# Kernel optimization log

Hardware: AMD Instinct MI355X
Metric: run time of the kernel (lower is better)

Reference implementation:

```python
import jax, jax.numpy as jnp
import numpy as np

B, T, D = 2, 2048, 2048
H = 16
DK = 64          # head_k_dim (key_dim = D*0.5 = 1024)
DV = 128         # head_v_dim (value_dim = D*1.0 = 2048)
R = 16           # gate_low_rank_dim
GLN = 16.0       # gate_logit_normalizer
C = 64           # chunk size
EPS = 1e-5


def setup_inputs() -> dict:
    key = jax.random.key(0)
    ks = jax.random.split(key, 12)
    s = 0.02
    return {
        "hidden_states": jax.random.normal(ks[0], (B, T, D), jnp.float32),
        "Wq": jax.random.normal(ks[1], (D, H * DK), jnp.float32) * s,
        "Wk": jax.random.normal(ks[2], (D, H * DK), jnp.float32) * s,
        "Wv": jax.random.normal(ks[3], (D, H * DV), jnp.float32) * s,
        "Wgk1": jax.random.normal(ks[4], (D, R), jnp.float32) * s,
        "Wgk2": jax.random.normal(ks[5], (R, H * DK), jnp.float32) * s,
        "bgk2": jnp.zeros((H * DK,), jnp.float32),
        "Wg1": jax.random.normal(ks[6], (D, R), jnp.float32) * s,
        "Wg2": jax.random.normal(ks[7], (R, H * DV), jnp.float32) * s,
        "bg2": jnp.zeros((H * DV,), jnp.float32),
        "Wo": jax.random.normal(ks[8], (H * DV, D), jnp.float32) * s,
        "gnorm_w": jnp.ones((DV,), jnp.float32),
    }


def _gla_chunk(q, k, v, gk):
    """Chunked gated linear attention.
    q,k,gk: [B,T,H,DK], v: [B,T,H,DV]. Recurrence:
    S_t = diag(exp(gk_t)) S_{t-1} + k_t v_t^T ; o_t = q_t @ S_t.
    """
    nC = T // C
    # [nC, B, H, C, d]
    def to_chunks(x):
        return x.reshape(B, nC, C, H, -1).transpose(1, 0, 3, 2, 4)
    qc, kc, vc, gkc = map(to_chunks, (q, k, v, gk))
    Gc = jnp.cumsum(gkc, axis=3)  # inclusive cumsum of log-decays within chunk
    tri = jnp.tril(jnp.ones((C, C), bool))

    def step(S, inp):
        q_c, k_c, v_c, G_c = inp  # [B,H,C,dk] / [B,H,C,dv]
        qg = q_c * jnp.exp(G_c)            # decays <= 0 within chunk -> safe
        kg = k_c * jnp.exp(-G_c)
        # inter-chunk: state contribution
        o = jnp.einsum('bhcd,bhde->bhce', qg, S)
        # intra-chunk causal attention with decay
        A = jnp.einsum('bhid,bhjd->bhij', qg, kg)
        A = jnp.where(tri, A, 0.0)
        o = o + jnp.einsum('bhij,bhje->bhie', A, v_c)
        # state update
        G_last = G_c[:, :, -1, :]                       # [B,H,dk]
        k_dec = k_c * jnp.exp(G_last[:, :, None, :] - G_c)
        S = S * jnp.exp(G_last)[:, :, :, None] + jnp.einsum('bhcd,bhce->bhde', k_dec, v_c)
        return S, o

    S0 = jnp.zeros((B, H, DK, DV), q.dtype)
    _, o = jax.lax.scan(step, S0, (qc, kc, vc, Gc))
    # [nC,B,H,C,dv] -> [B,T,H,dv]
    return o.transpose(1, 0, 3, 2, 4).reshape(B, T, H, DV)


def reference(hidden_states, Wq, Wk, Wv, Wgk1, Wgk2, bgk2, Wg1, Wg2, bg2, Wo, gnorm_w):
    hs = hidden_states
    q = jax.nn.silu(hs @ Wq).reshape(B, T, H, DK)
    k = jax.nn.silu(hs @ Wk).reshape(B, T, H, DK)
    v = jax.nn.silu(hs @ Wv).reshape(B, T, H, DV)
    gk = ((hs @ Wgk1) @ Wgk2 + bgk2).reshape(B, T, H, DK)
    gk = jax.nn.log_sigmoid(gk) / GLN
    q = q * (DK ** -0.5)  # fla default scale
    o = _gla_chunk(q, k, v, gk)  # [B,T,H,DV]
    # RMSNorm over head_v_dim
    o = o * jax.lax.rsqrt(jnp.mean(o * o, axis=-1, keepdims=True) + EPS) * gnorm_w
    g = ((hs @ Wg1) @ Wg2 + bg2).reshape(B, T, H, DV)
    o = o * jax.nn.sigmoid(g)
    return o.reshape(B, T, H * DV) @ Wo
```

## Files before the change

kernel.cpp:

```cpp
#include <hip/hip_runtime.h>
#include <cstdint>

#define Bq   2
#define Tq   2048
#define Dq   2048
#define Hq   16
#define DKq  64
#define DVq  128
#define Cq   64
#define NCq  32
#define Mq   4096
#define NBH  32

typedef _Float16 f16;
typedef f16 f16x4 __attribute__((ext_vector_type(4)));
typedef f16 f16x8 __attribute__((ext_vector_type(8)));
typedef float f32x4 __attribute__((ext_vector_type(4)));
typedef unsigned short u16;
typedef u16 u16x8 __attribute__((ext_vector_type(8)));

__device__ __forceinline__ void gl_lds16(const void* g, void* l) {
    __builtin_amdgcn_global_load_lds(
        (const __attribute__((address_space(1))) uint32_t*)g,
        (__attribute__((address_space(3))) uint32_t*)l, 16, 0, 0);
}

#define BARX()   asm volatile("s_barrier" ::: "memory")
#define LGKM0()  asm volatile("s_waitcnt lgkmcnt(0)" ::: "memory")
#define VMW8()   asm volatile("s_waitcnt vmcnt(8)" ::: "memory")
#define VMW6()   asm volatile("s_waitcnt vmcnt(6)" ::: "memory")

__global__ __launch_bounds__(256) void trans_all(const float* __restrict__ Wq,
                                                 const float* __restrict__ Wk,
                                                 const float* __restrict__ Wv,
                                                 const float* __restrict__ Wo,
                                                 f16* __restrict__ Qkv, f16* __restrict__ WoT) {
    __shared__ float sh[4096];
    int blk = blockIdx.x;
    int tid = threadIdx.x;
    const float* W; f16* Dh; int N, nt, kt; long rowoff;
    if (blk < 2048)      { W = Wq; N = 1024; int t = blk;        nt = t & 31; kt = t >> 5; Dh = Qkv; rowoff = 0; }
    else if (blk < 4096) { W = Wk; N = 1024; int t = blk - 2048; nt = t & 31; kt = t >> 5; Dh = Qkv; rowoff = 1024; }
    else if (blk < 8192) { W = Wv; N = 2048; int t = blk - 4096; nt = t & 63; kt = t >> 6; Dh = Qkv; rowoff = 2048; }
    else                 { W = Wo; N = 2048; int t = blk - 8192; nt = t & 63; kt = t >> 6; Dh = WoT; rowoff = 0; }
    int tx = tid & 31, ty = tid >> 5;
#pragma unroll
    for (int i = 0; i < 4; i++) {
        int k = kt * 32 + ty + i * 8;
        int n = nt * 32 + tx;
        sh[tx * 33 + ty + i * 8] = W[(long)k * N + n];
    }
    __syncthreads();
#pragma unroll
    for (int i = 0; i < 4; i++) {
        int n = nt * 32 + ty + i * 8;
        int k = kt * 32 + tx;
        Dh[(rowoff + n) * 2048L + k] = (f16)sh[(ty + i * 8) * 33 + tx];
    }
}

__global__ __launch_bounds__(256) void hs_conv(const float* __restrict__ in,
                                               f16* __restrict__ out) {
    long i = ((long)blockIdx.x * 256 + threadIdx.x) * 8;
    float4 a = *(const float4*)(in + i);
    float4 b = *(const float4*)(in + i + 4);
    f16x8 h;
    h[0] = (f16)a.x; h[1] = (f16)a.y; h[2] = (f16)a.z; h[3] = (f16)a.w;
    h[4] = (f16)b.x; h[5] = (f16)b.y; h[6] = (f16)b.z; h[7] = (f16)b.w;
    *(f16x8*)(out + i) = h;
}

__global__ __launch_bounds__(256) void lowrank_tg(const float* __restrict__ hs,
                                                  const float* __restrict__ Wgk1,
                                                  const float* __restrict__ Wg1,
                                                  float* __restrict__ t_gk,
                                                  float* __restrict__ t_g) {
    __shared__ float sW[512 * 32];
    int tid = threadIdx.x;
    int blk = blockIdx.x;
    int r = tid >> 4, seg = tid & 15;
    long row = (long)blk * 16 + r;
    float acc[32];
#pragma unroll
    for (int c = 0; c < 32; c++) acc[c] = 0.f;
    for (int kc = 0; kc < 2048; kc += 512) {
        __syncthreads();
#pragma unroll
        for (int i = 0; i < 16; i++) {
            int s = tid + i * 256;
            int k = s >> 3, q = s & 7;
            float4 w = (q < 4) ? *(const float4*)(Wgk1 + (long)(kc + k) * 16 + q * 4)
                               : *(const float4*)(Wg1  + (long)(kc + k) * 16 + (q - 4) * 4);
            int qs = q ^ ((k >> 5) & 7);
            *(float4*)&sW[k * 32 + qs * 4] = w;
        }
        __syncthreads();
        const float* hp = hs + row * 2048 + kc + seg * 32;
        int xr = seg & 7;
#pragma unroll
        for (int k4 = 0; k4 < 8; k4++) {
            float4 hv = *(const float4*)(hp + k4 * 4);
            float hvv[4] = {hv.x, hv.y, hv.z, hv.w};
#pragma unroll
            for (int u = 0; u < 4; u++) {
                int k = seg * 32 + k4 * 4 + u;
                const float* wr = &sW[k * 32];
#pragma unroll
                for (int q = 0; q < 8; q++) {
                    float4 wv = *(const float4*)(wr + ((q ^ xr) * 4));
                    acc[q * 4 + 0] += hvv[u] * wv.x;
                    acc[q * 4 + 1] += hvv[u] * wv.y;
                    acc[q * 4 + 2] += hvv[u] * wv.z;
                    acc[q * 4 + 3] += hvv[u] * wv.w;
                }
            }
        }
    }
#pragma unroll
    for (int c = 0; c < 32; c++) {
        acc[c] += __shfl_xor(acc[c], 1);
        acc[c] += __shfl_xor(acc[c], 2);
        acc[c] += __shfl_xor(acc[c], 4);
        acc[c] += __shfl_xor(acc[c], 8);
    }
    if (seg == 0) {
        float4 a;
        a.x = acc[0];  a.y = acc[1];  a.z = acc[2];  a.w = acc[3];  *(float4*)(t_gk + row * 16)     = a;
        a.x = acc[4];  a.y = acc[5];  a.z = acc[6];  a.w = acc[7];  *(float4*)(t_gk + row * 16 + 4) = a;
        a.x = acc[8];  a.y = acc[9];  a.z = acc[10]; a.w = acc[11]; *(float4*)(t_gk + row * 16 + 8) = a;
        a.x = acc[12]; a.y = acc[13]; a.z = acc[14]; a.w = acc[15]; *(float4*)(t_gk + row * 16 + 12)= a;
        a.x = acc[16]; a.y = acc[17]; a.z = acc[18]; a.w = acc[19]; *(float4*)(t_g + row * 16)      = a;
        a.x = acc[20]; a.y = acc[21]; a.z = acc[22]; a.w = acc[23]; *(float4*)(t_g + row * 16 + 4)  = a;
        a.x = acc[24]; a.y = acc[25]; a.z = acc[26]; a.w = acc[27]; *(float4*)(t_g + row * 16 + 8)  = a;
        a.x = acc[28]; a.y = acc[29]; a.z = acc[30]; a.w = acc[31]; *(float4*)(t_g + row * 16 + 12) = a;
    }
}

__global__ __launch_bounds__(512, 2) void gemm256q(const f16* __restrict__ A,
                                                   const f16* __restrict__ Bt,
                                                   f16* __restrict__ h0,
                                                   f16* __restrict__ h1,
                                                   f16* __restrict__ h2) {
    __shared__ __align__(16) f16 sA[2][16384];
    __shared__ __align__(16) f16 sB[2][16384];
    int tid = threadIdx.x;
    int wave = tid >> 6, lane = tid & 63;
    int quad = lane >> 4, l16 = lane & 15;
    int wm = wave >> 2, wn = wave & 3;

    int cpx = (int)gridDim.x >> 3;
    int wid = ((int)blockIdx.x & 7) * cpx + ((int)blockIdx.x >> 3);
    int bm = wid & 15, bn = wid >> 4;

    const f16* Ab = A  + (long)bm * 256 * 2048;
    const f16* Bb = Bt + (long)bn * 256 * 2048;

    int srow = tid >> 3;
    int gsrc = ((tid & 7) ^ (srow & 7)) * 8;
    const f16* Asrc = Ab + (long)srow * 2048 + gsrc;
    const f16* Bsrc = Bb + (long)srow * 2048 + gsrc;

#define STAGE(P, KT) do { \
    const f16* as_ = Asrc + (KT) * 64; \
    const f16* bs_ = Bsrc + (KT) * 64; \
    f16* la_ = &sA[P][tid * 8]; \
    f16* lb_ = &sB[P][tid * 8]; \
    _Pragma("unroll") \
    for (int q_ = 0; q_ < 4; q_++) gl_lds16(as_ + (long)q_ * 64 * 2048, la_ + q_ * 4096); \
    _Pragma("unroll") \
    for (int q_ = 0; q_ < 4; q_++) gl_lds16(bs_ + (long)q_ * 64 * 2048, lb_ + q_ * 4096); \
} while (0)

    int go0 = (quad ^ (l16 & 7)) * 8;
    int go1 = go0 ^ 32;
    const f16* aB0 = &sA[0][(wm * 128 + l16) * 64];
    const f16* aB1 = &sA[1][(wm * 128 + l16) * 64];
    const f16* bB0 = &sB[0][(wn * 64 + l16) * 64];
    const f16* bB1 = &sB[1][(wn * 64 + l16) * 64];

    f16x8 afr[4][2], bfr[2][2][2];
    f32x4 acc[8][4] = {};

#define LDA(PB, MH) do { \
    _Pragma("unroll") \
    for (int ii_ = 0; ii_ < 4; ii_++) { \
        afr[ii_][0] = *(const f16x8*)(PB + ((MH) * 4 + ii_) * 1024 + go0); \
        afr[ii_][1] = *(const f16x8*)(PB + ((MH) * 4 + ii_) * 1024 + go1); \
    } \
} while (0)

#define LDB(PB, NH) do { \
    _Pragma("unroll") \
    for (int jj_ = 0; jj_ < 2; jj_++) { \
        bfr[NH][jj_][0] = *(const f16x8*)(PB + ((NH) * 2 + jj_) * 1024 + go0); \
        bfr[NH][jj_][1] = *(const f16x8*)(PB + ((NH) * 2 + jj_) * 1024 + go1); \
    } \
} while (0)

#define QMFMA(MH, NH) do { \
    __builtin_amdgcn_s_setprio(1); \
    _Pragma("unroll") \
    for (int ii_ = 0; ii_ < 4; ii_++) \
    _Pragma("unroll") \
    for (int jj_ = 0; jj_ < 2; jj_++) { \
        acc[(MH)*4+ii_][(NH)*2+jj_] = __builtin_amdgcn_mfma_f32_16x16x32_f16(afr[ii_][0], bfr[NH][jj_][0], acc[(MH)*4+ii_][(NH)*2+jj_], 0, 0, 0); \
        acc[(MH)*4+ii_][(NH)*2+jj_] = __builtin_amdgcn_mfma_f32_16x16x32_f16(afr[ii_][1], bfr[NH][jj_][1], acc[(MH)*4+ii_][(NH)*2+jj_], 0, 0, 0); \
    } \
    __builtin_amdgcn_s_setprio(0); \
} while (0)

    STAGE(0, 0);
    STAGE(1, 1);
    VMW8();
    BARX();

#pragma unroll 1
    for (int it = 0; it < 16; it++) {
        int kt2 = 2 * it + 2; if (kt2 > 31) kt2 = 31;
        int kt3 = 2 * it + 3; if (kt3 > 31) kt3 = 31;
        LDA(aB0, 0); LDB(bB0, 0);
        BARX(); LGKM0(); QMFMA(0, 0); BARX();
        LDB(bB0, 1);
        BARX(); LGKM0(); QMFMA(0, 1); BARX();
        LDA(aB0, 1);
        BARX(); LGKM0(); QMFMA(1, 0); BARX();
        STAGE(0, kt2);
        VMW8();
        BARX(); QMFMA(1, 1); BARX();
        LDA(aB1, 0); LDB(bB1, 0);
        BARX(); LGKM0(); QMFMA(0, 0); BARX();
        LDB(bB1, 1);
        BARX(); LGKM0(); QMFMA(0, 1); BARX();
        LDA(aB1, 1);
        BARX(); LGKM0(); QMFMA(1, 0); BARX();
        STAGE(1, kt3);
        VMW8();
        BARX(); QMFMA(1, 1); BARX();
    }
    asm volatile("s_waitcnt vmcnt(0)" ::: "memory");

    long rb = (long)bm * 256 + wm * 128 + quad * 4;
    f16* dst; long cw, cb; float sc = 1.f;
    if (bn < 4)      { dst = h0; cw = 1024; cb = (long)bn * 256;       sc = 0.125f; }
    else if (bn < 8) { dst = h1; cw = 1024; cb = (long)(bn - 4) * 256; }
    else             { dst = h2; cw = 2048; cb = (long)(bn - 8) * 256; }
    long cbase = cb + wn * 64 + l16;
#pragma unroll
    for (int i = 0; i < 8; i++)
#pragma unroll
        for (int j = 0; j < 4; j++)
#pragma unroll
            for (int r = 0; r < 4; r++) {
                float x = acc[i][j][r];
                x = x / (1.f + __expf(-x)) * sc;
                dst[(rb + i * 16 + r) * cw + cbase + j * 16] = (f16)x;
            }
#undef STAGE
#undef LDA
#undef LDB
#undef QMFMA
}

__global__ __launch_bounds__(512, 2) void gemm128o(const f16* __restrict__ A,
                                                   const f16* __restrict__ Bt,
                                                   float* __restrict__ o0) {
    __shared__ __align__(16) f16 sAb[16384];
    __shared__ __align__(16) f16 sBb[32768];
    int tid = threadIdx.x;
    int wave = tid >> 6, lane = tid & 63;
    int quad = lane >> 4, l16 = lane & 15;
    int wm = wave >> 2, wn = wave & 3;

    int cpx = (int)gridDim.x >> 3;
    int wid = ((int)blockIdx.x & 7) * cpx + ((int)blockIdx.x >> 3);
    int bm = wid & 31, bn = wid >> 5;

    int srow = tid >> 3;
    int gsrc = ((tid & 7) ^ (srow & 7)) * 8;
    const f16* Asrc = A  + ((long)bm * 128 + srow) * 2048 + gsrc;
    const f16* Bsrc = Bt + ((long)bn * 256 + srow) * 2048 + gsrc;

#define STAGE(P, KT) do { \
    _Pragma("unroll") \
    for (int q_ = 0; q_ < 2; q_++) \
        gl_lds16(Asrc + (KT) * 64 + (long)q_ * 64 * 2048, sAb + (P) * 8192 + tid * 8 + q_ * 4096); \
    _Pragma("unroll") \
    for (int q_ = 0; q_ < 4; q_++) \
        gl_lds16(Bsrc + (KT) * 64 + (long)q_ * 64 * 2048, sBb + (P) * 16384 + tid * 8 + q_ * 4096); \
} while (0)

    int go0 = (quad ^ (l16 & 7)) * 8;
    int go1 = go0 ^ 32;
    const f16* pA0 = sAb + (wm * 64 + l16) * 64 + go0;
    const f16* pA1 = sAb + (wm * 64 + l16) * 64 + go1;
    const f16* pB0 = sBb + (wn * 64 + l16) * 64 + go0;
    const f16* pB1 = sBb + (wn * 64 + l16) * 64 + go1;

    f16x8 aX[4], bX[4], aY[4], bY[4];
    f32x4 acc[4][4] = {};

#define RDA(D, PTR, POFF) do { \
    D[0] = *(const f16x8*)((PTR) + (POFF)); \
    D[1] = *(const f16x8*)((PTR) + (POFF) + 1024); \
    D[2] = *(const f16x8*)((PTR) + (POFF) + 2048); \
    D[3] = *(const f16x8*)((PTR) + (POFF) + 3072); \
} while (0)

#define MM(AS, BS) do { \
    __builtin_amdgcn_s_setprio(1); \
    _Pragma("unroll") \
    for (int m_ = 0; m_ < 4; m_++) \
    _Pragma("unroll") \
    for (int n_ = 0; n_ < 4; n_++) \
        acc[m_][n_] = __builtin_amdgcn_mfma_f32_16x16x32_f16(AS[m_], BS[n_], acc[m_][n_], 0, 0, 0); \
    __builtin_amdgcn_s_setprio(0); \
} while (0)

    STAGE(0, 0);
    STAGE(1, 1);
    VMW6();
    BARX();
    RDA(aX, pA0, 0); RDA(bX, pB0, 0);

#pragma unroll 1
    for (int it = 0; it < 16; it++) {
        int c2 = 2 * it + 2; if (c2 > 31) c2 = 31;
        int c3 = 2 * it + 3; if (c3 > 31) c3 = 31;
        RDA(aY, pA1, 0); RDA(bY, pB1, 0);
        MM(aX, bX);
        LGKM0();
        BARX();
        STAGE(0, c2);
        VMW6();
        BARX();
        RDA(aX, pA0, 8192); RDA(bX, pB0, 16384);
        MM(aY, bY);
        RDA(aY, pA1, 8192); RDA(bY, pB1, 16384);
        MM(aX, bX);
        LGKM0();
        BARX();
        STAGE(1, c3);
        VMW6();
        BARX();
        RDA(aX, pA0, 0); RDA(bX, pB0, 0);
        MM(aY, bY);
    }
    asm volatile("s_waitcnt vmcnt(0)" ::: "memory");

    long rb = (long)bm * 128 + wm * 64 + quad * 4;
    long cbase = (long)bn * 256 + wn * 64 + l16;
#pragma unroll
    for (int m = 0; m < 4; m++)
#pragma unroll
        for (int n = 0; n < 4; n++)
#pragma unroll
            for (int r = 0; r < 4; r++)
                o0[(rb + m * 16 + r) * 2048 + cbase + n * 16] = acc[m][n][r];
#undef STAGE
#undef RDA
#undef MM
}

__global__ __launch_bounds__(256) void vtrans(const u16* __restrict__ v,
                                              u16* __restrict__ vT) {
    __shared__ uint32_t su[128 * 65];
    int tid = threadIdx.x;
    int t0 = (blockIdx.x >> 5) * 128;
    int e0 = (blockIdx.x & 31) * 64;
#pragma unroll
    for (int i = 0; i < 4; i++) {
        int tr = i * 32 + (tid >> 3);
        int ec = (tid & 7) * 8;
        u16x8 g = *(const u16x8*)(v + (long)(t0 + tr) * 2048 + e0 + ec);
#pragma unroll
        for (int j = 0; j < 8; j++) su[tr * 65 + ec + j] = g[j];
    }
    __syncthreads();
#pragma unroll
    for (int i = 0; i < 2; i++) {
        int er = i * 32 + (tid >> 3);
        int tch = (tid & 7) * 16;
        u16x8 o0, o1;
#pragma unroll
        for (int j = 0; j < 8; j++) {
            o0[j] = (u16)su[(tch + j) * 65 + er];
            o1[j] = (u16)su[(tch + 8 + j) * 65 + er];
        }
        u16* dst = vT + (long)(e0 + er) * 4096 + t0 + tch;
        *(u16x8*)dst = o0;
        *(u16x8*)(dst + 8) = o1;
    }
}

__global__ __launch_bounds__(256) void gk_cum(const float* __restrict__ t_gk,
                                              const float* __restrict__ Wgk2,
                                              const float* __restrict__ bgk2,
                                              float* __restrict__ G,
                                              float* __restrict__ dec) {
    __shared__ float sT[1024];
    __shared__ float sW[1024];
    __shared__ float sb[64];
    __shared__ float sG[64 * 64];
    int blk = blockIdx.x;
    int c = blk & 31, h = (blk >> 5) & 15, b = blk >> 9;
    int tid = threadIdx.x;
    long rowbase = (long)b * Tq + c * 64;
    {
        int idx = tid * 4;
        *(float4*)&sT[idx] = *(const float4*)(t_gk + rowbase * 16 + idx);
        int rr = idx >> 6, dd = idx & 63;
        *(float4*)&sW[idx] = *(const float4*)(Wgk2 + rr * 1024 + h * 64 + dd);
    }
    if (tid < 64) sb[tid] = bgk2[h * 64 + tid];
    __syncthreads();
    int tquad = tid >> 4, dgrp = tid & 15;
    float4 bg4 = *(float4*)&sb[dgrp * 4];
#pragma unroll
    for (int j = 0; j < 4; j++) {
        int t = tquad * 4 + j;
        float4 z = bg4;
#pragma unroll
        for (int rr = 0; rr < 16; rr++) {
            float tv = sT[t * 16 + rr];
            float4 wv = *(float4*)&sW[rr * 64 + dgrp * 4];
            z.x += tv * wv.x; z.y += tv * wv.y; z.z += tv * wv.z; z.w += tv * wv.w;
        }
        float4 o;
        o.x = (fminf(z.x, 0.f) - log1pf(__expf(-fabsf(z.x)))) * 0.0625f;
        o.y = (fminf(z.y, 0.f) - log1pf(__expf(-fabsf(z.y)))) * 0.0625f;
        o.z = (fminf(z.z, 0.f) - log1pf(__expf(-fabsf(z.z)))) * 0.0625f;
        o.w = (fminf(z.w, 0.f) - log1pf(__expf(-fabsf(z.w)))) * 0.0625f;
        *(float4*)&sG[t * 64 + dgrp * 4] = o;
    }
    __syncthreads();
    if (tid < 64) {
        float run = 0.f;
        for (int t = 0; t < 64; t++) { run += sG[t * 64 + tid]; sG[t * 64 + tid] = run; }
        dec[blk * 64 + tid] = __expf(run);
    }
    __syncthreads();
    float* Gb = G + (long)blk * 4096;
#pragma unroll
    for (int i = 0; i < 4; i++) {
        int f = tid + i * 256;
        *(float4*)(Gb + f * 4) = *(float4*)&sG[f * 4];
    }
}

#define ST 68
__global__ __launch_bounds__(256) void gla_pass1(const f16* __restrict__ kbuf,
                                                 const f16* __restrict__ vh,
                                                 const float* __restrict__ G,
                                                 float* __restrict__ U) {
    __shared__ float sG[64 * ST];
    __shared__ float sK[64 * ST];
    int blk = blockIdx.x;
    int c = blk & 31, h = (blk >> 5) & 15, b = blk >> 9;
    int tid = threadIdx.x;
    long rowbase = (long)b * Tq + c * 64;
    const float* Gb = G + (long)blk * 4096;
#pragma unroll
    for (int i = 0; i < 4; i++) {
        int f = tid + i * 256;
        float4 v = *(const float4*)(Gb + f * 4);
        int t = f >> 4, d0 = (f & 15) * 4;
        *(float4*)&sG[t * ST + d0] = v;
    }
    __syncthreads();
#pragma unroll
    for (int i = 0; i < 16; i++) {
        int idx = tid + i * 256;
        int t = idx >> 6, d = idx & 63;
        float gl = sG[63 * ST + d];
        sK[t * ST + d] = (float)kbuf[(rowbase + t) * 1024 + h * 64 + d] * __expf(gl - sG[t * ST + d]);
    }
    __syncthreads();
    int ty = tid >> 4, tx = tid & 15;
    float acc[4][8] = {};
    const f16* vb = vh + rowbase * 2048 + h * 128 + tx * 8;
    for (int t = 0; t < 64; t++) {
        float kd[4];
        *(float4*)&kd[0] = *(float4*)&sK[t * ST + ty * 4];
        f16x8 vv = *(const f16x8*)(vb + (long)t * 2048);
        float ve[8];
#pragma unroll
        for (int e = 0; e < 8; e++) ve[e] = (float)vv[e];
#pragma unroll
        for (int r = 0; r < 4; r++)
#pragma unroll
            for (int e = 0; e < 8; e++) acc[r][e] += kd[r] * ve[e];
    }
    float* Ub = U + (long)blk * 8192;
#pragma unroll
    for (int r = 0; r < 4; r++) {
        int d = ty * 4 + r;
#pragma unroll
        for (int e8 = 0; e8 < 8; e8++)
            Ub[(tx * 8 + e8) * 64 + d] = acc[r][e8];
    }
}

__global__ __launch_bounds__(256) void gla_pass2(const float* __restrict__ U,
                                                 const float* __restrict__ dec,
                                                 f16* __restrict__ ShT) {
    int bh = blockIdx.x >> 2;
    int tid = threadIdx.x;
    int e = (blockIdx.x & 3) * 32 + (tid >> 3);
    int d0 = (tid & 7) * 8;
    float4 Sa = {0.f, 0.f, 0.f, 0.f}, Sb = {0.f, 0.f, 0.f, 0.f};
    for (int c = 0; c < NCq; c++) {
        long base = ((long)(bh * 32 + c) * 128 + e) * 64 + d0;
        float4 u0 = *(const float4*)(U + base);
        float4 u1 = *(const float4*)(U + base + 4);
        const float* dp = dec + (bh * 32 + c) * 64 + d0;
        float4 dc0 = *(const float4*)dp;
        float4 dc1 = *(const float4*)(dp + 4);
        f16x8 sh;
        sh[0] = (f16)Sa.x; sh[1] = (f16)Sa.y; sh[2] = (f16)Sa.z; sh[3] = (f16)Sa.w;
        sh[4] = (f16)Sb.x; sh[5] = (f16)Sb.y; sh[6] = (f16)Sb.z; sh[7] = (f16)Sb.w;
        *(f16x8*)(ShT + base) = sh;
        Sa.x = Sa.x * dc0.x + u0.x; Sa.y = Sa.y * dc0.y + u0.y;
        Sa.z = Sa.z * dc0.z + u0.z; Sa.w = Sa.w * dc0.w + u0.w;
        Sb.x = Sb.x * dc1.x + u1.x; Sb.y = Sb.y * dc1.y + u1.y;
        Sb.z = Sb.z * dc1.z + u1.z; Sb.w = Sb.w * dc1.w + u1.w;
    }
}

#define GRD(row, kslot) (((row) << 6) + ((((kslot) ^ ((row) & 7))) << 3))
__global__ __launch_bounds__(256) void gla_pass3(const f16* __restrict__ qb,
                                                 const f16* __restrict__ kb,
                                                 const float* __restrict__ G,
                                                 const float* __restrict__ t_g,
                                                 const float* __restrict__ Wg2,
                                                 const float* __restrict__ bg2,
                                                 const float* __restrict__ gnw,
                                                 const f16* __restrict__ ShT,
                                                 const f16* __restrict__ vT,
                                                 f16* __restrict__ Oh) {
    __shared__ __align__(16) f16 sQg[4096];
    __shared__ __align__(16) f16 sKg[4096];
    __shared__ __align__(16) f16 sAh[4096];
    __shared__ __align__(16) f16 sST[8192];
    __shared__ __align__(16) f16 sVT[8192];
    __shared__ float sWg[16 * 128];
    __shared__ float sbg[128];
    int blk = blockIdx.x;
    int c = blk & 31, h = (blk >> 5) & 15, b = blk >> 9;
    int tid = threadIdx.x;
    long rowbase = (long)b * Tq + c * 64;

#pragma unroll
    for (int i = 0; i < 4; i++) {
        int s = tid + i * 256;
        int e = s >> 3, gp = s & 7;
        int gl = gp ^ (e & 7);
        gl_lds16(ShT + (long)blk * 8192 + e * 64 + gl * 8, sST + s * 8);
        gl_lds16(vT + (long)(h * 128 + e) * 4096 + rowbase + gl * 8, sVT + s * 8);
    }
#pragma unroll
    for (int i = 0; i < 2; i++) {
        int idx = tid * 4 + i * 1024;
        int rr = idx >> 7, ee = idx & 127;
        *(float4*)&sWg[idx] = *(const float4*)(Wg2 + (long)rr * 2048 + h * 128 + ee);
    }
    if (tid < 128) sbg[tid] = bg2[h * 128 + tid];
#pragma unroll
    for (int i = 0; i < 4; i++) {
        int f = tid + i * 256;
        int t = f >> 4, gi = f & 15;
        float4 G4 = *(const float4*)(G + (long)blk * 4096 + f * 4);
        long gb = (rowbase + t) * 1024 + h * 64 + gi * 4;
        f16x4 q4 = *(const f16x4*)(qb + gb);
        f16x4 k4 = *(const f16x4*)(kb + gb);
        f16x4 qh, kh;
        float ex;
        ex = __expf(G4.x); qh[0] = (f16)((float)q4[0] * ex); kh[0] = (f16)((float)k4[0] / ex);
        ex = __expf(G4.y); qh[1] = (f16)((float)q4[1] * ex); kh[1] = (f16)((float)k4[1] / ex);
        ex = __expf(G4.z); qh[2] = (f16)((float)q4[2] * ex); kh[2] = (f16)((float)k4[2] / ex);
        ex = __expf(G4.w); qh[3] = (f16)((float)q4[3] * ex); kh[3] = (f16)((float)k4[3] / ex);
        int w = (t << 6) + ((((gi >> 1) ^ (t & 7))) << 3) + ((gi & 1) << 2);
        *(f16x4*)(sQg + w) = qh;
        *(f16x4*)(sKg + w) = kh;
    }
    __syncthreads();

    int wv = tid >> 6, lane = tid & 63;
    int quad = lane >> 4, l16 = lane & 15;
    int trow = wv * 16 + l16;

    f16x8 afq[2];
    afq[0] = *(const f16x8*)(sQg + GRD(trow, quad));
    afq[1] = *(const f16x8*)(sQg + GRD(trow, 4 + quad));
#pragma unroll
    for (int j4 = 0; j4 < 4; j4++) {
        int tc = j4 * 16 + l16;
        f16x8 bk0 = *(const f16x8*)(sKg + GRD(tc, quad));
        f16x8 bk1 = *(const f16x8*)(sKg + GRD(tc, 4 + quad));
        f32x4 ca = {};
        ca = __builtin_amdgcn_mfma_f32_16x16x32_f16(afq[0], bk0, ca, 0, 0, 0);
        ca = __builtin_amdgcn_mfma_f32_16x16x32_f16(afq[1], bk1, ca, 0, 0, 0);
#pragma unroll
        for (int r = 0; r < 4; r++) {
            int tr = wv * 16 + quad * 4 + r;
            int tcw = j4 * 16 + l16;
            f16 av = (tcw <= tr) ? (f16)ca[r] : (f16)0.f;
            sAh[(tr << 6) + ((((tcw >> 3) ^ (tr & 7))) << 3) + (tcw & 7)] = av;
        }
    }

    f16x8 afa[2];
    afa[0] = *(const f16x8*)(sAh + GRD(trow, quad));
    afa[1] = *(const f16x8*)(sAh + GRD(trow, 4 + quad));
    f32x4 acc[8];
#pragma unroll
    for (int et = 0; et < 8; et++) {
        int e = et * 16 + l16;
        f16x8 bs0 = *(const f16x8*)(sST + GRD(e, quad));
        f16x8 bs1 = *(const f16x8*)(sST + GRD(e, 4 + quad));
        f16x8 bv0 = *(const f16x8*)(sVT + GRD(e, quad));
        f16x8 bv1 = *(const f16x8*)(sVT + GRD(e, 4 + quad));
        f32x4 cc = {};
        cc = __builtin_amdgcn_mfma_f32_16x16x32_f16(afq[0], bs0, cc, 0, 0, 0);
        cc = __builtin_amdgcn_mfma_f32_16x16x32_f16(afq[1], bs1, cc, 0, 0, 0);
        cc = __builtin_amdgcn_mfma_f32_16x16x32_f16(afa[0], bv0, cc, 0, 0, 0);
        cc = __builtin_amdgcn_mfma_f32_16x16x32_f16(afa[1], bv1, cc, 0, 0, 0);
        acc[et] = cc;
    }

    float gw[8], bgv[8];
#pragma unroll
    for (int et = 0; et < 8; et++) {
        gw[et]  = gnw[et * 16 + l16];
        bgv[et] = sbg[et * 16 + l16];
    }
#pragma unroll
    for (int half = 0; half < 2; half++) {
        float tg[2][16];
#pragma unroll
        for (int rh = 0; rh < 2; rh++) {
            int t = wv * 16 + quad * 4 + half * 2 + rh;
            const float* tgp = t_g + (rowbase + t) * 16;
#pragma unroll
            for (int q4 = 0; q4 < 4; q4++)
                *(float4*)&tg[rh][q4 * 4] = *(const float4*)(tgp + q4 * 4);
        }
        float g[2][8];
#pragma unroll
        for (int rh = 0; rh < 2; rh++)
#pragma unroll
            for (int et = 0; et < 8; et++) g[rh][et] = bgv[et];
#pragma unroll
        for (int rr = 0; rr < 16; rr++) {
#pragma unroll
            for (int et = 0; et < 8; et++) {
                float wv_ = sWg[rr * 128 + et * 16 + l16];
                g[0][et] += tg[0][rr] * wv_;
                g[1][et] += tg[1][rr] * wv_;
            }
        }
#pragma unroll
        for (int rh = 0; rh < 2; rh++) {
            int r = half * 2 + rh;
            int t = wv * 16 + quad * 4 + r;
            float ss = 0.f;
#pragma unroll
            for (int et = 0; et < 8; et++) ss += acc[et][r] * acc[et][r];
            ss += __shfl_xor(ss, 1);
            ss += __shfl_xor(ss, 2);
            ss += __shfl_xor(ss, 4);
            ss += __shfl_xor(ss, 8);
            float scale = rsqrtf(ss * (1.f / 128.f) + 1e-5f);
            long off = (rowbase + t) * 2048 + h * 128 + l16;
#pragma unroll
            for (int et = 0; et < 8; et++) {
                float y = acc[et][r] * scale * gw[et] / (1.f + __expf(-g[rh][et]));
                Oh[off + et * 16] = (f16)y;
            }
        }
    }
}

extern "C" void kernel_launch(void* const* d_in, const int* in_sizes, int n_in,
                              void* d_out, int out_size, void* d_ws, size_t ws_size,
                              hipStream_t stream) {
    const float* hs   = (const float*)d_in[0];
    const float* Wq   = (const float*)d_in[1];
    const float* Wk   = (const float*)d_in[2];
    const float* Wv   = (const float*)d_in[3];
    const float* Wgk1 = (const float*)d_in[4];
    const float* Wgk2 = (const float*)d_in[5];
    const float* bgk2 = (const float*)d_in[6];
    const float* Wg1  = (const float*)d_in[7];
    const float* Wg2  = (const float*)d_in[8];
    const float* bg2  = (const float*)d_in[9];
    const float* Wo   = (const float*)d_in[10];
    const float* gnw  = (const float*)d_in[11];

    char* w = (char*)d_ws;
    auto alloc = [&](size_t bytes) {
        char* p = w; w += (bytes + 255) & ~size_t(255); return (void*)p;
    };
    f16*   Xh     = (f16*)  alloc((size_t)Mq * Dq * 2);
    f16*   WqkvT  = (f16*)  alloc((size_t)4224 * 2048 * 2);
    f16*   WoT    = (f16*)  alloc((size_t)2048 * 2048 * 2);
    f16*   qb     = (f16*)  alloc((size_t)Mq * 1024 * 2);
    f16*   kb     = (f16*)  alloc((size_t)Mq * 1024 * 2);
    f16*   vhb    = (f16*)  alloc((size_t)Mq * 2048 * 2);
    f16*   vTb    = (f16*)  alloc((size_t)Mq * 2048 * 2);
    float* t_gk   = (float*)alloc((size_t)Mq * 16 * 4);
    float* t_g    = (float*)alloc((size_t)Mq * 16 * 4);
    float* Ut     = (float*)alloc((size_t)NBH * NCq * 8192 * 4);
    f16*   ShT    = (f16*)  alloc((size_t)NBH * NCq * 8192 * 2);
    float* dec    = (float*)alloc((size_t)NBH * NCq * 64 * 4);
    float* Gbuf   = (float*)alloc((size_t)NBH * NCq * 4096 * 4);

    trans_all<<<12288, 256, 0, stream>>>(Wq, Wk, Wv, Wo, WqkvT, WoT);
    hs_conv<<<Mq * Dq / 2048, 256, 0, stream>>>(hs, Xh);
    lowrank_tg<<<256, 256, 0, stream>>>(hs, Wgk1, Wg1, t_gk, t_g);

    gemm256q<<<256, 512, 0, stream>>>(Xh, WqkvT, qb, kb, vhb);
    vtrans<<<1024, 256, 0, stream>>>((const u16*)vhb, (u16*)vTb);

    gk_cum<<<NBH * NCq, 256, 0, stream>>>(t_gk, Wgk2, bgk2, Gbuf, dec);
    gla_pass1<<<NBH * NCq, 256, 0, stream>>>(kb, vhb, Gbuf, Ut);
    gla_pass2<<<NBH * 4, 256, 0, stream>>>(Ut, dec, ShT);
    gla_pass3<<<NBH * NCq, 256, 0, stream>>>(qb, kb, Gbuf, t_g, Wg2, bg2, gnw, ShT, vTb, Xh);

    gemm128o<<<256, 512, 0, stream>>>(Xh, WoT, (float*)d_out);
}
```

Baseline: 396.6 us.

## Use MFMA for chunk state updates, widen weight transpose tiles, split state scan finer

The per-chunk k_dec^T·V product in gla_pass1 now runs on 16x16x32 f16 MFMA instructions. It reads V from the transposed buffer into swizzled LDS via direct global-to-LDS loads and stores the decayed K in f16, where it was previously an fp32 scalar FMA loop. The weight transpose kernel moves to 64x64 tiles with float4 reads and 8-wide f16 writes, cutting the block count fourfold. gla_pass2 splits the sequential scan across twice as many blocks with 4-wide vectors to raise parallelism. Rounding decayed K to f16 adds some precision loss in the state.

```diff
diff --git a/kernel.cpp b/kernel.cpp
--- a/kernel.cpp
+++ b/kernel.cpp
@@ -35,27 +35,34 @@
                                                  const float* __restrict__ Wv,
                                                  const float* __restrict__ Wo,
                                                  f16* __restrict__ Qkv, f16* __restrict__ WoT) {
-    __shared__ float sh[4096];
+    __shared__ float sh[64 * 65];
     int blk = blockIdx.x;
     int tid = threadIdx.x;
     const float* W; f16* Dh; int N, nt, kt; long rowoff;
-    if (blk < 2048)      { W = Wq; N = 1024; int t = blk;        nt = t & 31; kt = t >> 5; Dh = Qkv; rowoff = 0; }
-    else if (blk < 4096) { W = Wk; N = 1024; int t = blk - 2048; nt = t & 31; kt = t >> 5; Dh = Qkv; rowoff = 1024; }
-    else if (blk < 8192) { W = Wv; N = 2048; int t = blk - 4096; nt = t & 63; kt = t >> 6; Dh = Qkv; rowoff = 2048; }
-    else                 { W = Wo; N = 2048; int t = blk - 8192; nt = t & 63; kt = t >> 6; Dh = WoT; rowoff = 0; }
-    int tx = tid & 31, ty = tid >> 5;
-#pragma unroll
-    for (int i = 0; i < 4; i++) {
-        int k = kt * 32 + ty + i * 8;
-        int n = nt * 32 + tx;
-        sh[tx * 33 + ty + i * 8] = W[(long)k * N + n];
+    if (blk < 512)       { W = Wq; N = 1024; int t = blk;        nt = t & 15; kt = t >> 4; Dh = Qkv; rowoff = 0; }
+    else if (blk < 1024) { W = Wk; N = 1024; int t = blk - 512;  nt = t & 15; kt = t >> 4; Dh = Qkv; rowoff = 1024; }
+    else if (blk < 2048) { W = Wv; N = 2048; int t = blk - 1024; nt = t & 31; kt = t >> 5; Dh = Qkv; rowoff = 2048; }
+    else                 { W = Wo; N = 2048; int t = blk - 2048; nt = t & 31; kt = t >> 5; Dh = WoT; rowoff = 0; }
+    int k0 = kt * 64, n0 = nt * 64;
+    int kr = tid >> 4, nc = (tid & 15) * 4;
+#pragma unroll
+    for (int p = 0; p < 4; p++) {
+        int k = kr + p * 16;
+        float4 w4 = *(const float4*)(W + (long)(k0 + k) * N + n0 + nc);
+        sh[(nc + 0) * 65 + k] = w4.x;
+        sh[(nc + 1) * 65 + k] = w4.y;
+        sh[(nc + 2) * 65 + k] = w4.z;
+        sh[(nc + 3) * 65 + k] = w4.w;
     }
     __syncthreads();
-#pragma unroll
-    for (int i = 0; i < 4; i++) {
-        int n = nt * 32 + ty + i * 8;
-        int k = kt * 32 + tx;
-        Dh[(rowoff + n) * 2048L + k] = (f16)sh[(ty + i * 8) * 33 + tx];
+    int nr = tid >> 3, kch = (tid & 7) * 8;
+#pragma unroll
+    for (int p = 0; p < 2; p++) {
+        int n = nr + p * 32;
+        f16x8 o;
+#pragma unroll
+        for (int j = 0; j < 8; j++) o[j] = (f16)sh[n * 65 + kch + j];
+        *(f16x8*)(Dh + (rowoff + n0 + n) * 2048L + k0 + kch) = o;
     }
 }
 
@@ -447,86 +454,95 @@
     }
 }
 
-#define ST 68
-__global__ __launch_bounds__(256) void gla_pass1(const f16* __restrict__ kbuf,
-                                                 const f16* __restrict__ vh,
+#define GRD(row, kslot) (((row) << 6) + ((((kslot) ^ ((row) & 7))) << 3))
+__global__ __launch_bounds__(256) void gla_pass1(const f16* __restrict__ kb,
+                                                 const f16* __restrict__ vT,
                                                  const float* __restrict__ G,
                                                  float* __restrict__ U) {
-    __shared__ float sG[64 * ST];
-    __shared__ float sK[64 * ST];
+    __shared__ __align__(16) f16 sKd[4096];
+    __shared__ __align__(16) f16 sVT[8192];
     int blk = blockIdx.x;
     int c = blk & 31, h = (blk >> 5) & 15, b = blk >> 9;
     int tid = threadIdx.x;
     long rowbase = (long)b * Tq + c * 64;
-    const float* Gb = G + (long)blk * 4096;
+
+#pragma unroll
+    for (int i = 0; i < 4; i++) {
+        int s = tid + i * 256;
+        int e = s >> 3, gp = s & 7;
+        int gl = gp ^ (e & 7);
+        gl_lds16(vT + (long)(h * 128 + e) * 4096 + rowbase + gl * 8, sVT + s * 8);
+    }
 #pragma unroll
     for (int i = 0; i < 4; i++) {
         int f = tid + i * 256;
-        float4 v = *(const float4*)(Gb + f * 4);
-        int t = f >> 4, d0 = (f & 15) * 4;
-        *(float4*)&sG[t * ST + d0] = v;
+        int t = f >> 4, gi = f & 15;
+        int d0 = gi * 4;
+        float4 G4 = *(const float4*)(G + (long)blk * 4096 + f * 4);
+        float4 GL = *(const float4*)(G + (long)blk * 4096 + 63 * 64 + d0);
+        f16x4 k4 = *(const f16x4*)(kb + (rowbase + t) * 1024 + h * 64 + d0);
+        float kv[4];
+        kv[0] = (float)k4[0] * __expf(GL.x - G4.x);
+        kv[1] = (float)k4[1] * __expf(GL.y - G4.y);
+        kv[2] = (float)k4[2] * __expf(GL.z - G4.z);
+        kv[3] = (float)k4[3] * __expf(GL.w - G4.w);
+#pragma unroll
+        for (int j = 0; j < 4; j++) {
+            int d = d0 + j;
+            sKd[(d << 6) + ((((t >> 3) ^ (d & 7))) << 3) + (t & 7)] = (f16)kv[j];
+        }
     }
     __syncthreads();
-#pragma unroll
-    for (int i = 0; i < 16; i++) {
-        int idx = tid + i * 256;
-        int t = idx >> 6, d = idx & 63;
-        float gl = sG[63 * ST + d];
-        sK[t * ST + d] = (float)kbuf[(rowbase + t) * 1024 + h * 64 + d] * __expf(gl - sG[t * ST + d]);
-    }
-    __syncthreads();
-    int ty = tid >> 4, tx = tid & 15;
-    float acc[4][8] = {};
-    const f16* vb = vh + rowbase * 2048 + h * 128 + tx * 8;
-    for (int t = 0; t < 64; t++) {
-        float kd[4];
-        *(float4*)&kd[0] = *(float4*)&sK[t * ST + ty * 4];
-        f16x8 vv = *(const f16x8*)(vb + (long)t * 2048);
-        float ve[8];
-#pragma unroll
-        for (int e = 0; e < 8; e++) ve[e] = (float)vv[e];
-#pragma unroll
-        for (int r = 0; r < 4; r++)
-#pragma unroll
-            for (int e = 0; e < 8; e++) acc[r][e] += kd[r] * ve[e];
+
+    int wv = tid >> 6, lane = tid & 63;
+    int quad = lane >> 4, l16 = lane & 15;
+
+    f16x8 bk[4][2];
+#pragma unroll
+    for (int dt = 0; dt < 4; dt++) {
+        int d = dt * 16 + l16;
+        bk[dt][0] = *(const f16x8*)(sKd + GRD(d, quad));
+        bk[dt][1] = *(const f16x8*)(sKd + GRD(d, 4 + quad));
     }
     float* Ub = U + (long)blk * 8192;
 #pragma unroll
-    for (int r = 0; r < 4; r++) {
-        int d = ty * 4 + r;
-#pragma unroll
-        for (int e8 = 0; e8 < 8; e8++)
-            Ub[(tx * 8 + e8) * 64 + d] = acc[r][e8];
+    for (int es = 0; es < 2; es++) {
+        int e = wv * 32 + es * 16 + l16;
+        f16x8 av0 = *(const f16x8*)(sVT + GRD(e, quad));
+        f16x8 av1 = *(const f16x8*)(sVT + GRD(e, 4 + quad));
+        int erow = wv * 32 + es * 16 + quad * 4;
+#pragma unroll
+        for (int dt = 0; dt < 4; dt++) {
+            f32x4 cc = {};
+            cc = __builtin_amdgcn_mfma_f32_16x16x32_f16(av0, bk[dt][0], cc, 0, 0, 0);
+            cc = __builtin_amdgcn_mfma_f32_16x16x32_f16(av1, bk[dt][1], cc, 0, 0, 0);
+#pragma unroll
+            for (int r = 0; r < 4; r++)
+                Ub[(erow + r) * 64 + dt * 16 + l16] = cc[r];
+        }
     }
 }
 
 __global__ __launch_bounds__(256) void gla_pass2(const float* __restrict__ U,
                                                  const float* __restrict__ dec,
                                                  f16* __restrict__ ShT) {
-    int bh = blockIdx.x >> 2;
-    int tid = threadIdx.x;
-    int e = (blockIdx.x & 3) * 32 + (tid >> 3);
-    int d0 = (tid & 7) * 8;
-    float4 Sa = {0.f, 0.f, 0.f, 0.f}, Sb = {0.f, 0.f, 0.f, 0.f};
+    int bh = blockIdx.x >> 3;
+    int tid = threadIdx.x;
+    int e = (blockIdx.x & 7) * 16 + (tid >> 4);
+    int d0 = (tid & 15) * 4;
+    float4 Sa = {0.f, 0.f, 0.f, 0.f};
     for (int c = 0; c < NCq; c++) {
         long base = ((long)(bh * 32 + c) * 128 + e) * 64 + d0;
         float4 u0 = *(const float4*)(U + base);
-        float4 u1 = *(const float4*)(U + base + 4);
-        const float* dp = dec + (bh * 32 + c) * 64 + d0;
-        float4 dc0 = *(const float4*)dp;
-        float4 dc1 = *(const float4*)(dp + 4);
-        f16x8 sh;
+        float4 dc0 = *(const float4*)(dec + (bh * 32 + c) * 64 + d0);
+        f16x4 sh;
         sh[0] = (f16)Sa.x; sh[1] = (f16)Sa.y; sh[2] = (f16)Sa.z; sh[3] = (f16)Sa.w;
-        sh[4] = (f16)Sb.x; sh[5] = (f16)Sb.y; sh[6] = (f16)Sb.z; sh[7] = (f16)Sb.w;
-        *(f16x8*)(ShT + base) = sh;
+        *(f16x4*)(ShT + base) = sh;
         Sa.x = Sa.x * dc0.x + u0.x; Sa.y = Sa.y * dc0.y + u0.y;
         Sa.z = Sa.z * dc0.z + u0.z; Sa.w = Sa.w * dc0.w + u0.w;
-        Sb.x = Sb.x * dc1.x + u1.x; Sb.y = Sb.y * dc1.y + u1.y;
-        Sb.z = Sb.z * dc1.z + u1.z; Sb.w = Sb.w * dc1.w + u1.w;
-    }
-}
-
-#define GRD(row, kslot) (((row) << 6) + ((((kslot) ^ ((row) & 7))) << 3))
+    }
+}
+
 __global__ __launch_bounds__(256) void gla_pass3(const f16* __restrict__ qb,
                                                  const f16* __restrict__ kb,
                                                  const float* __restrict__ G,
@@ -714,7 +730,7 @@
     float* dec    = (float*)alloc((size_t)NBH * NCq * 64 * 4);
     float* Gbuf   = (float*)alloc((size_t)NBH * NCq * 4096 * 4);
 
-    trans_all<<<12288, 256, 0, stream>>>(Wq, Wk, Wv, Wo, WqkvT, WoT);
+    trans_all<<<3072, 256, 0, stream>>>(Wq, Wk, Wv, Wo, WqkvT, WoT);
     hs_conv<<<Mq * Dq / 2048, 256, 0, stream>>>(hs, Xh);
     lowrank_tg<<<256, 256, 0, stream>>>(hs, Wgk1, Wg1, t_gk, t_g);
 
@@ -722,8 +738,8 @@
     vtrans<<<1024, 256, 0, stream>>>((const u16*)vhb, (u16*)vTb);
 
     gk_cum<<<NBH * NCq, 256, 0, stream>>>(t_gk, Wgk2, bgk2, Gbuf, dec);
-    gla_pass1<<<NBH * NCq, 256, 0, stream>>>(kb, vhb, Gbuf, Ut);
-    gla_pass2<<<NBH * 4, 256, 0, stream>>>(Ut, dec, ShT);
+    gla_pass1<<<NBH * NCq, 256, 0, stream>>>(kb, vTb, Gbuf, Ut);
+    gla_pass2<<<NBH * 8, 256, 0, stream>>>(Ut, dec, ShT);
     gla_pass3<<<NBH * NCq, 256, 0, stream>>>(qb, kb, Gbuf, t_g, Wg2, bg2, gnw, ShT, vTb, Xh);
 
     gemm128o<<<256, 512, 0, stream>>>(Xh, WoT, (float*)d_out);
```

New measurement: 407.7 us. 2.8% more time.
